# Kernel optimization log

Measured on AMD Instinct MI355X. Metric: run time of the kernel, lower is better.

## Reference

```python
import jax, jax.numpy as jnp
import numpy as np

SCALE = 16.0 / 8  # alpha / rank

def setup_inputs() -> dict:
    key = jax.random.key(0)
    k1, k2, k3, k4 = jax.random.split(key, 4)
    B, S, D_IN, D_OUT, R = 4, 2048, 4096, 4096, 8
    x = jax.random.normal(k1, (B, S, D_IN), dtype=jnp.float32)
    weight = jax.random.normal(k2, (D_OUT, D_IN), dtype=jnp.float32) * (1.0 / np.sqrt(D_IN))
    lora_A = jax.random.normal(k3, (R, D_IN), dtype=jnp.float32) * (1.0 / np.sqrt(D_IN))
    lora_B = jax.random.normal(k4, (D_OUT, R), dtype=jnp.float32) * 0.01
    return {"x": x, "weight": weight, "lora_A": lora_A, "lora_B": lora_B}

def reference(x, weight, lora_A, lora_B):
    # base: x @ W^T  -> [B, S, out]
    base_out = jnp.einsum('bsd,od->bso', x, weight)
    # low-rank path, chained as (x @ A^T) @ B^T (same math as x @ (B@A)^T)
    xa = jnp.einsum('bsd,rd->bsr', x, lora_A)      # [B, S, r]
    lora_out = jnp.einsum('bsr,or->bso', xa, lora_B)  # [B, S, out]
    return base_out + SCALE * lora_out
```

## Files before the change

kernel.cpp:

```cpp
#include <hip/hip_runtime.h>
#include <hip/hip_bf16.h>

typedef unsigned short u16;
typedef __attribute__((ext_vector_type(8))) __bf16 bf16x8;
typedef __attribute__((ext_vector_type(4))) float f32x4;
typedef __attribute__((ext_vector_type(8))) unsigned short ushort8;

#define GM 8192
#define GN 4096
#define GK 4096
#define NT (GK / 64)

__device__ __forceinline__ u16 f2bf(float f) {
  unsigned u = __float_as_uint(f);
  u += 0x7fffu + ((u >> 16) & 1u);
  return (u16)(u >> 16);
}

__global__ void build_weff(const float* __restrict__ W,
                           const float* __restrict__ lA,
                           const float* __restrict__ lB,
                           u16* __restrict__ Weff) {
  const int o = blockIdx.x;
  float b[8];
#pragma unroll
  for (int r = 0; r < 8; ++r) b[r] = 2.0f * lB[o * 8 + r];
  const float* wrow = W + (size_t)o * GK;
  u16* orow = Weff + (size_t)o * GK;
  for (int d = threadIdx.x * 4; d < GK; d += blockDim.x * 4) {
    float4 w = *reinterpret_cast<const float4*>(wrow + d);
    float a0 = w.x, a1 = w.y, a2 = w.z, a3 = w.w;
#pragma unroll
    for (int r = 0; r < 8; ++r) {
      float4 a = *reinterpret_cast<const float4*>(lA + r * GK + d);
      a0 += b[r] * a.x; a1 += b[r] * a.y; a2 += b[r] * a.z; a3 += b[r] * a.w;
    }
    ushort4 p;
    p.x = f2bf(a0); p.y = f2bf(a1); p.z = f2bf(a2); p.w = f2bf(a3);
    *reinterpret_cast<ushort4*>(orow + d) = p;
  }
}

__global__ void cvt_bf16(const float* __restrict__ x, u16* __restrict__ xb) {
  const size_t i = ((size_t)blockIdx.x * blockDim.x + threadIdx.x) * 8;
  float4 v0 = *reinterpret_cast<const float4*>(x + i);
  float4 v1 = *reinterpret_cast<const float4*>(x + i + 4);
  ushort8 o;
  o[0] = f2bf(v0.x); o[1] = f2bf(v0.y); o[2] = f2bf(v0.z); o[3] = f2bf(v0.w);
  o[4] = f2bf(v1.x); o[5] = f2bf(v1.y); o[6] = f2bf(v1.z); o[7] = f2bf(v1.w);
  *reinterpret_cast<ushort8*>(xb + i) = o;
}

__device__ __forceinline__ void gload16(const u16* g, u16* l) {
  __builtin_amdgcn_global_load_lds(
      (const __attribute__((address_space(1))) void*)g,
      (__attribute__((address_space(3))) void*)l, 16, 0, 0);
}

#define BAR()                                  \
  do {                                         \
    asm volatile("" ::: "memory");             \
    __builtin_amdgcn_s_barrier();              \
    asm volatile("" ::: "memory");             \
  } while (0)

__global__ __launch_bounds__(512, 2) void gemm256(const u16* __restrict__ Ab,
                                                  const u16* __restrict__ Bb,
                                                  float* __restrict__ C) {
  __shared__ u16 lds[2][2][256 * 64];

  const int tid = threadIdx.x;
  const int wv = tid >> 6;
  const int l = tid & 63;

  const int nwg = gridDim.x;
  const int cpx = nwg >> 3;
  const int wg = ((int)blockIdx.x & 7) * cpx + ((int)blockIdx.x >> 3);
  const int tm = wg >> 4;
  const int tn = wg & 15;

  const int wr = wv >> 2;
  const int wc = wv & 3;

  const int srow = (wv << 3) + (l >> 3);
  const int srl = ((wv & 1) << 3) | (l >> 3);
  const int skel = ((l & 7) << 3) ^ ((srl & 0xE) << 2);
  const u16* aG = Ab + (size_t)(tm * 256) * GK;
  const u16* bG = Bb + (size_t)(tn * 256) * GK;

  const int frow = l & 15;
  const int fksw = ((l >> 4) << 3) ^ ((frow & 0xE) << 2);
  const int arow = wr * 128 + frow;
  const int brow = wc * 64 + frow;

  auto STAGE = [&](int th, int r) {
    const int k0 = th << 6;
    const u16* src = (r < 2 ? aG : bG) +
                     (size_t)((r & 1) * 128 + srow) * GK + k0 + skel;
    u16* dst = &lds[th & 1][r >> 1][(r & 1) * 8192 + wv * 512];
#pragma unroll
    for (int j = 0; j < 2; ++j)
      gload16(src + (size_t)(j * 64) * GK, dst + j * 4096);
  };

  STAGE(0, 0); STAGE(0, 1); STAGE(0, 2); STAGE(0, 3);
  STAGE(1, 2); STAGE(1, 0); STAGE(1, 1);

  f32x4 acc[8][4] = {};
  bf16x8 af[8][2], bfr[4][2];

  asm volatile("s_waitcnt vmcnt(6)" ::: "memory");
  BAR();

  for (int t = 0; t < NT; ++t) {
    const u16* A = &lds[t & 1][0][0];
    const u16* B = &lds[t & 1][1][0];
#pragma unroll
    for (int q = 0; q < 4; ++q) {
      if (q == 0) {
#pragma unroll
        for (int n = 0; n < 4; ++n)
#pragma unroll
          for (int s = 0; s < 2; ++s)
            bfr[n][s] = *reinterpret_cast<const bf16x8*>(
                B + (brow + n * 16) * 64 + (fksw ^ (s << 5)));
#pragma unroll
        for (int m = 0; m < 2; ++m)
#pragma unroll
          for (int s = 0; s < 2; ++s)
            af[m][s] = *reinterpret_cast<const bf16x8*>(
                A + (arow + m * 16) * 64 + (fksw ^ (s << 5)));
      } else if (q == 1) {
#pragma unroll
        for (int m = 2; m < 8; ++m)
#pragma unroll
          for (int s = 0; s < 2; ++s)
            af[m][s] = *reinterpret_cast<const bf16x8*>(
                A + (arow + m * 16) * 64 + (fksw ^ (s << 5)));
      }
      if (q == 0) { if (t + 1 < NT) STAGE(t + 1, 3); }
      else if (q == 1) { if (t + 2 < NT) STAGE(t + 2, 2); }
      else if (q == 2) { if (t + 2 < NT) STAGE(t + 2, 0); }
      else { if (t + 2 < NT) STAGE(t + 2, 1); }

      BAR();
      __builtin_amdgcn_s_setprio(1);
#pragma unroll
      for (int mm = 0; mm < 2; ++mm) {
#pragma unroll
        for (int n = 0; n < 4; ++n)
#pragma unroll
          for (int s = 0; s < 2; ++s)
            acc[2 * q + mm][n] = __builtin_amdgcn_mfma_f32_16x16x32_bf16(
                af[2 * q + mm][s], bfr[n][s], acc[2 * q + mm][n], 0, 0, 0);
      }
      __builtin_amdgcn_s_setprio(0);
      if (q == 3) {
        if (t < NT - 2)
          asm volatile("s_waitcnt vmcnt(6)" ::: "memory");
        else if (t == NT - 2)
          asm volatile("s_waitcnt vmcnt(0)" ::: "memory");
      }
      BAR();
    }
  }

  const int orow = tm * 256 + wr * 128 + ((l >> 4) << 2);
  const int ocol = tn * 256 + wc * 64 + (l & 15);
#pragma unroll
  for (int m = 0; m < 8; ++m)
#pragma unroll
    for (int n = 0; n < 4; ++n) {
      float* cp = C + (size_t)(orow + m * 16) * GN + (ocol + n * 16);
#pragma unroll
      for (int j = 0; j < 4; ++j) cp[(size_t)j * GN] = acc[m][n][j];
    }
}

extern "C" void kernel_launch(void* const* d_in, const int* in_sizes, int n_in,
                              void* d_out, int out_size, void* d_ws, size_t ws_size,
                              hipStream_t stream) {
  const float* x  = (const float*)d_in[0];
  const float* W  = (const float*)d_in[1];
  const float* lA = (const float*)d_in[2];
  const float* lB = (const float*)d_in[3];
  float* out = (float*)d_out;

  u16* weff = (u16*)d_ws;
  u16* xb = (u16*)((char*)d_ws + (size_t)GN * GK * sizeof(u16));

  build_weff<<<GN, 256, 0, stream>>>(W, lA, lB, weff);
  cvt_bf16<<<(size_t)GM * GK / (256 * 8), 256, 0, stream>>>(x, xb);
  gemm256<<<(GM / 256) * (GN / 256), 512, 0, stream>>>(xb, weff, out);
}
```

Baseline: 309.6 us.

## Fuse prep kernels and replace 256-tile GEMM with simpler 128-tile double-buffered GEMM

Merges the weight-merge and x-to-bf16 conversion kernels into a single launch, each thread now converting 16 elements of x. The GEMM drops its 256x256 tile, 8-wave, quarter-step pipelined schedule for a 128x128 tile with 4 waves and simple double buffering: wait for all loads, barrier, read fragments, issue the next tile's loads, then run the MFMAs. The aim is to cut a launch and gain more workgroups and occupancy. In exchange it lowers data reuse per tile, doubling the global and LDS traffic per FLOP, and serialises load waits with compute more coarsely.

```diff
diff --git a/kernel.cpp b/kernel.cpp
--- a/kernel.cpp
+++ b/kernel.cpp
@@ -17,38 +17,45 @@
   return (u16)(u >> 16);
 }
 
-__global__ void build_weff(const float* __restrict__ W,
-                           const float* __restrict__ lA,
-                           const float* __restrict__ lB,
-                           u16* __restrict__ Weff) {
-  const int o = blockIdx.x;
-  float b[8];
+__global__ void prep(const float* __restrict__ W,
+                     const float* __restrict__ lA,
+                     const float* __restrict__ lB,
+                     u16* __restrict__ Weff,
+                     const float* __restrict__ x,
+                     u16* __restrict__ xb) {
+  const int bid = blockIdx.x;
+  if (bid < GN) {
+    const int o = bid;
+    float b[8];
 #pragma unroll
-  for (int r = 0; r < 8; ++r) b[r] = 2.0f * lB[o * 8 + r];
-  const float* wrow = W + (size_t)o * GK;
-  u16* orow = Weff + (size_t)o * GK;
-  for (int d = threadIdx.x * 4; d < GK; d += blockDim.x * 4) {
-    float4 w = *reinterpret_cast<const float4*>(wrow + d);
-    float a0 = w.x, a1 = w.y, a2 = w.z, a3 = w.w;
+    for (int r = 0; r < 8; ++r) b[r] = 2.0f * lB[o * 8 + r];
+    const float* wrow = W + (size_t)o * GK;
+    u16* orow = Weff + (size_t)o * GK;
+    for (int d = threadIdx.x * 4; d < GK; d += blockDim.x * 4) {
+      float4 w = *reinterpret_cast<const float4*>(wrow + d);
+      float a0 = w.x, a1 = w.y, a2 = w.z, a3 = w.w;
 #pragma unroll
-    for (int r = 0; r < 8; ++r) {
-      float4 a = *reinterpret_cast<const float4*>(lA + r * GK + d);
-      a0 += b[r] * a.x; a1 += b[r] * a.y; a2 += b[r] * a.z; a3 += b[r] * a.w;
+      for (int r = 0; r < 8; ++r) {
+        float4 a = *reinterpret_cast<const float4*>(lA + r * GK + d);
+        a0 += b[r] * a.x; a1 += b[r] * a.y; a2 += b[r] * a.z; a3 += b[r] * a.w;
+      }
+      ushort4 p;
+      p.x = f2bf(a0); p.y = f2bf(a1); p.z = f2bf(a2); p.w = f2bf(a3);
+      *reinterpret_cast<ushort4*>(orow + d) = p;
     }
-    ushort4 p;
-    p.x = f2bf(a0); p.y = f2bf(a1); p.z = f2bf(a2); p.w = f2bf(a3);
-    *reinterpret_cast<ushort4*>(orow + d) = p;
+  } else {
+    const size_t base = ((size_t)(bid - GN) * 256 + threadIdx.x) * 16;
+#pragma unroll
+    for (int h = 0; h < 2; ++h) {
+      const size_t i = base + h * 8;
+      float4 v0 = *reinterpret_cast<const float4*>(x + i);
+      float4 v1 = *reinterpret_cast<const float4*>(x + i + 4);
+      ushort8 o;
+      o[0] = f2bf(v0.x); o[1] = f2bf(v0.y); o[2] = f2bf(v0.z); o[3] = f2bf(v0.w);
+      o[4] = f2bf(v1.x); o[5] = f2bf(v1.y); o[6] = f2bf(v1.z); o[7] = f2bf(v1.w);
+      *reinterpret_cast<ushort8*>(xb + i) = o;
+    }
   }
-}
-
-__global__ void cvt_bf16(const float* __restrict__ x, u16* __restrict__ xb) {
-  const size_t i = ((size_t)blockIdx.x * blockDim.x + threadIdx.x) * 8;
-  float4 v0 = *reinterpret_cast<const float4*>(x + i);
-  float4 v1 = *reinterpret_cast<const float4*>(x + i + 4);
-  ushort8 o;
-  o[0] = f2bf(v0.x); o[1] = f2bf(v0.y); o[2] = f2bf(v0.z); o[3] = f2bf(v0.w);
-  o[4] = f2bf(v1.x); o[5] = f2bf(v1.y); o[6] = f2bf(v1.z); o[7] = f2bf(v1.w);
-  *reinterpret_cast<ushort8*>(xb + i) = o;
 }
 
 __device__ __forceinline__ void gload16(const u16* g, u16* l) {
@@ -64,10 +71,10 @@
     asm volatile("" ::: "memory");             \
   } while (0)
 
-__global__ __launch_bounds__(512, 2) void gemm256(const u16* __restrict__ Ab,
+__global__ __launch_bounds__(256, 2) void gemm128(const u16* __restrict__ Ab,
                                                   const u16* __restrict__ Bb,
                                                   float* __restrict__ C) {
-  __shared__ u16 lds[2][2][256 * 64];
+  __shared__ u16 lds[2][2][128 * 64];
 
   const int tid = threadIdx.x;
   const int wv = tid >> 6;
@@ -76,99 +83,76 @@
   const int nwg = gridDim.x;
   const int cpx = nwg >> 3;
   const int wg = ((int)blockIdx.x & 7) * cpx + ((int)blockIdx.x >> 3);
-  const int tm = wg >> 4;
-  const int tn = wg & 15;
+  const int tm = wg >> 5;
+  const int tn = wg & 31;
 
-  const int wr = wv >> 2;
-  const int wc = wv & 3;
+  const int wr = wv >> 1;
+  const int wc = wv & 1;
 
   const int srow = (wv << 3) + (l >> 3);
   const int srl = ((wv & 1) << 3) | (l >> 3);
   const int skel = ((l & 7) << 3) ^ ((srl & 0xE) << 2);
-  const u16* aG = Ab + (size_t)(tm * 256) * GK;
-  const u16* bG = Bb + (size_t)(tn * 256) * GK;
+  const u16* aG = Ab + (size_t)(tm * 128) * GK;
+  const u16* bG = Bb + (size_t)(tn * 128) * GK;
 
   const int frow = l & 15;
   const int fksw = ((l >> 4) << 3) ^ ((frow & 0xE) << 2);
-  const int arow = wr * 128 + frow;
+  const int arow = wr * 64 + frow;
   const int brow = wc * 64 + frow;
 
   auto STAGE = [&](int th, int r) {
-    const int k0 = th << 6;
-    const u16* src = (r < 2 ? aG : bG) +
-                     (size_t)((r & 1) * 128 + srow) * GK + k0 + skel;
-    u16* dst = &lds[th & 1][r >> 1][(r & 1) * 8192 + wv * 512];
+    const int tc = th < NT ? th : NT - 1;
+    const int k0 = tc << 6;
+    const u16* src = (r == 0 ? aG : bG) + (size_t)srow * GK + k0 + skel;
+    u16* dst = &lds[th & 1][r][wv * 512];
 #pragma unroll
-    for (int j = 0; j < 2; ++j)
-      gload16(src + (size_t)(j * 64) * GK, dst + j * 4096);
+    for (int j = 0; j < 4; ++j)
+      gload16(src + (size_t)(j * 32) * GK, dst + j * 2048);
   };
 
-  STAGE(0, 0); STAGE(0, 1); STAGE(0, 2); STAGE(0, 3);
-  STAGE(1, 2); STAGE(1, 0); STAGE(1, 1);
+  STAGE(0, 0); STAGE(0, 1);
 
-  f32x4 acc[8][4] = {};
-  bf16x8 af[8][2], bfr[4][2];
-
-  asm volatile("s_waitcnt vmcnt(6)" ::: "memory");
-  BAR();
+  f32x4 acc[4][4] = {};
+  bf16x8 af[4][2], bf[4][2];
 
   for (int t = 0; t < NT; ++t) {
+    asm volatile("s_waitcnt vmcnt(0)" ::: "memory");
+    BAR();
+
     const u16* A = &lds[t & 1][0][0];
     const u16* B = &lds[t & 1][1][0];
+
 #pragma unroll
-    for (int q = 0; q < 4; ++q) {
-      if (q == 0) {
+    for (int n = 0; n < 4; ++n)
 #pragma unroll
-        for (int n = 0; n < 4; ++n)
+      for (int s = 0; s < 2; ++s)
+        bf[n][s] = *reinterpret_cast<const bf16x8*>(
+            B + (brow + n * 16) * 64 + (fksw ^ (s << 5)));
 #pragma unroll
-          for (int s = 0; s < 2; ++s)
-            bfr[n][s] = *reinterpret_cast<const bf16x8*>(
-                B + (brow + n * 16) * 64 + (fksw ^ (s << 5)));
+    for (int m = 0; m < 4; ++m)
 #pragma unroll
-        for (int m = 0; m < 2; ++m)
+      for (int s = 0; s < 2; ++s)
+        af[m][s] = *reinterpret_cast<const bf16x8*>(
+            A + (arow + m * 16) * 64 + (fksw ^ (s << 5)));
+
+    STAGE(t + 1, 0); STAGE(t + 1, 1);
+
+    __builtin_amdgcn_s_setprio(1);
 #pragma unroll
-          for (int s = 0; s < 2; ++s)
-            af[m][s] = *reinterpret_cast<const bf16x8*>(
-                A + (arow + m * 16) * 64 + (fksw ^ (s << 5)));
-      } else if (q == 1) {
+    for (int m = 0; m < 4; ++m)
 #pragma unroll
-        for (int m = 2; m < 8; ++m)
+      for (int n = 0; n < 4; ++n)
 #pragma unroll
-          for (int s = 0; s < 2; ++s)
-            af[m][s] = *reinterpret_cast<const bf16x8*>(
-                A + (arow + m * 16) * 64 + (fksw ^ (s << 5)));
-      }
-      if (q == 0) { if (t + 1 < NT) STAGE(t + 1, 3); }
-      else if (q == 1) { if (t + 2 < NT) STAGE(t + 2, 2); }
-      else if (q == 2) { if (t + 2 < NT) STAGE(t + 2, 0); }
-      else { if (t + 2 < NT) STAGE(t + 2, 1); }
-
-      BAR();
-      __builtin_amdgcn_s_setprio(1);
-#pragma unroll
-      for (int mm = 0; mm < 2; ++mm) {
-#pragma unroll
-        for (int n = 0; n < 4; ++n)
-#pragma unroll
-          for (int s = 0; s < 2; ++s)
-            acc[2 * q + mm][n] = __builtin_amdgcn_mfma_f32_16x16x32_bf16(
-                af[2 * q + mm][s], bfr[n][s], acc[2 * q + mm][n], 0, 0, 0);
-      }
-      __builtin_amdgcn_s_setprio(0);
-      if (q == 3) {
-        if (t < NT - 2)
-          asm volatile("s_waitcnt vmcnt(6)" ::: "memory");
-        else if (t == NT - 2)
-          asm volatile("s_waitcnt vmcnt(0)" ::: "memory");
-      }
-      BAR();
-    }
+        for (int s = 0; s < 2; ++s)
+          acc[m][n] = __builtin_amdgcn_mfma_f32_16x16x32_bf16(
+              af[m][s], bf[n][s], acc[m][n], 0, 0, 0);
+    __builtin_amdgcn_s_setprio(0);
   }
 
-  const int orow = tm * 256 + wr * 128 + ((l >> 4) << 2);
-  const int ocol = tn * 256 + wc * 64 + (l & 15);
+  const int orow = tm * 128 + wr * 64 + ((l >> 4) << 2);
+  const int ocol = tn * 128 + wc * 64 + (l & 15);
 #pragma unroll
-  for (int m = 0; m < 8; ++m)
+  for (int m = 0; m < 4; ++m)
 #pragma unroll
     for (int n = 0; n < 4; ++n) {
       float* cp = C + (size_t)(orow + m * 16) * GN + (ocol + n * 16);
@@ -189,7 +173,6 @@
   u16* weff = (u16*)d_ws;
   u16* xb = (u16*)((char*)d_ws + (size_t)GN * GK * sizeof(u16));
 
-  build_weff<<<GN, 256, 0, stream>>>(W, lA, lB, weff);
-  cvt_bf16<<<(size_t)GM * GK / (256 * 8), 256, 0, stream>>>(x, xb);
-  gemm256<<<(GM / 256) * (GN / 256), 512, 0, stream>>>(xb, weff, out);
+  prep<<<GN + (GM * GK) / (256 * 16), 256, 0, stream>>>(W, lA, lB, weff, x, xb);
+  gemm128<<<(GM / 128) * (GN / 128), 256, 0, stream>>>(xb, weff, out);
 }
```

Result: slower. 340.5 us (+10.0%).
